# Performance work log

Measured on AMD Instinct MI355X. Metric: run time of the kernel, lower is better.

## Reference

```python
import jax, jax.numpy as jnp
import numpy as np

D_MODEL = 2048
NHEADS = 16
NOPE = 128
ROPE = 64
VDIM = 128
QLORA = 1536
KVLORA = 512
QHD = NOPE + ROPE  # 192
B, T = 1, 4096


def rms_norm(x, w):
    # torch.nn.RMSNorm with eps=None uses finfo(dtype).eps
    eps = jnp.finfo(x.dtype).eps
    var = jnp.mean(x * x, axis=-1, keepdims=True)
    return x * jax.lax.rsqrt(var + eps) * w


def rope_cos_sin(T, dim):
    freqs = 1.0 / (10000.0 ** (jnp.arange(0, dim, 2, dtype=jnp.float32) / dim))
    ang = jnp.arange(T, dtype=jnp.float32)[:, None] * freqs[None, :]  # (T, dim/2)
    return jnp.cos(ang), jnp.sin(ang)


def apply_rope(x, cos, sin):
    # interleaved RoPE: even/odd channel pairs rotated
    xe = x[..., 0::2]
    xo = x[..., 1::2]
    re = xe * cos - xo * sin
    ro = xo * cos + xe * sin
    return jnp.stack([re, ro], axis=-1).reshape(x.shape)


def setup_inputs() -> dict:
    key = jax.random.key(0)
    ks = jax.random.split(key, 6)
    s = 0.02
    return {
        "x": jax.random.normal(ks[0], (B, T, D_MODEL), jnp.float32),
        "Wqa": jax.random.normal(ks[1], (D_MODEL, QLORA), jnp.float32) * s,
        "q_ln_w": jnp.ones((QLORA,), jnp.float32),
        "Wqb": jax.random.normal(ks[2], (QLORA, NHEADS * QHD), jnp.float32) * s,
        "Wkva": jax.random.normal(ks[3], (D_MODEL, KVLORA + ROPE), jnp.float32) * s,
        "kv_ln_w": jnp.ones((KVLORA,), jnp.float32),
        "Wkvb": jax.random.normal(ks[4], (KVLORA, NHEADS * (NOPE + VDIM)), jnp.float32) * s,
        "Wo": jax.random.normal(ks[5], (NHEADS * VDIM, D_MODEL), jnp.float32) * s,
    }


def reference(x, Wqa, q_ln_w, Wqb, Wkva, kv_ln_w, Wkvb, Wo):
    Bx, Tx, _ = x.shape
    cos, sin = rope_cos_sin(Tx, ROPE)  # (T, ROPE/2)

    # Low-rank Q path
    q = rms_norm(x @ Wqa, q_ln_w) @ Wqb
    q = q.reshape(Bx, Tx, NHEADS, QHD).transpose(0, 2, 1, 3)  # (B,H,T,QHD)
    q_nope = q[..., :NOPE]
    q_rope = apply_rope(q[..., NOPE:], cos, sin)  # (B,H,T,ROPE)

    # Compressed KV path + shared rope key
    kv = x @ Wkva
    kv_c = kv[..., :KVLORA]  # (B,T,KVLORA) latent cache
    k_rope = apply_rope(kv[..., KVLORA:], cos, sin)  # (B,T,ROPE), head-shared

    kvb = (rms_norm(kv_c, kv_ln_w) @ Wkvb).reshape(Bx, Tx, NHEADS, NOPE + VDIM)
    k_nope = kvb[..., :NOPE].transpose(0, 2, 1, 3)  # (B,H,T,NOPE)
    v = kvb[..., NOPE:].transpose(0, 2, 1, 3)       # (B,H,T,VDIM)

    # Scores split into nope part + head-shared rope part (avoids expanding k_rope to H heads)
    scale = 1.0 / jnp.sqrt(jnp.float32(QHD))
    s = jnp.einsum('bhqd,bhkd->bhqk', q_nope, k_nope)
    s = s + jnp.einsum('bhqd,bkd->bhqk', q_rope, k_rope)
    s = s * scale

    mask = jnp.tril(jnp.ones((Tx, Tx), dtype=bool))
    s = jnp.where(mask, s, -jnp.inf)
    a = jax.nn.softmax(s, axis=-1)

    o = jnp.einsum('bhqk,bhkd->bhqd', a, v)
    o = o.transpose(0, 2, 1, 3).reshape(Bx, Tx, NHEADS * VDIM)
    return o @ Wo
```

## Files before the change

### kernel.cpp

```cpp
#include <hip/hip_runtime.h>
#include <hip/hip_bf16.h>

typedef __attribute__((ext_vector_type(8))) short short8;
typedef __attribute__((ext_vector_type(4))) float f32x4;

#define GLDS16(gp, lp)                                                         \
  __builtin_amdgcn_global_load_lds(                                            \
      (const __attribute__((address_space(1))) void*)(gp),                     \
      (__attribute__((address_space(3))) void*)(lp), 16, 0, 0)

static __device__ __forceinline__ unsigned int pack_bf16(float a, float b) {
  __hip_bfloat16 ba = __float2bfloat16(a), bb = __float2bfloat16(b);
  unsigned short ua = *reinterpret_cast<unsigned short*>(&ba);
  unsigned short ub = *reinterpret_cast<unsigned short*>(&bb);
  return (unsigned int)ua | ((unsigned int)ub << 16);
}

static __device__ __forceinline__ int xcd_swz(int linear, int nwg) {
  return (linear & 7) * (nwg >> 3) + (linear >> 3);
}

__global__ __launch_bounds__(256) void cast_bf16_kernel(
    const float* __restrict__ in, __hip_bfloat16* __restrict__ out, int n4)
{
  int i = blockIdx.x * 256 + threadIdx.x;
  if (i < n4) {
    float4 v = ((const float4*)in)[i];
    out[(size_t)i * 4 + 0] = __float2bfloat16(v.x);
    out[(size_t)i * 4 + 1] = __float2bfloat16(v.y);
    out[(size_t)i * 4 + 2] = __float2bfloat16(v.z);
    out[(size_t)i * 4 + 3] = __float2bfloat16(v.w);
  }
}

__global__ void transpose_cast_kernel(const float* __restrict__ in,
                                      __hip_bfloat16* __restrict__ out,
                                      int K, int N, int Npad)
{
  __shared__ float tile[32][33];
  int n0 = blockIdx.x * 32, k0 = blockIdx.y * 32;
  int tx = threadIdx.x, ty = threadIdx.y;
  #pragma unroll
  for (int i = ty; i < 32; i += 8) {
    int k = k0 + i, n = n0 + tx;
    tile[i][tx] = (n < N) ? in[(size_t)k * N + n] : 0.f;
  }
  __syncthreads();
  #pragma unroll
  for (int i = ty; i < 32; i += 8) {
    int n = n0 + i, k = k0 + tx;
    if (n < Npad) out[(size_t)n * K + k] = __float2bfloat16(tile[tx][i]);
  }
}

__global__ void rope_tab_kernel(float* __restrict__ cs, float* __restrict__ sn)
{
  int t = blockIdx.x, i = threadIdx.x;
  float freq = powf(10000.f, -2.f * (float)i / 64.f);
  float ang = (float)t * freq;
  cs[t * 32 + i] = cosf(ang);
  sn[t * 32 + i] = sinf(ang);
}

#define GEMM_MAIN(A, BT, Kdim)                                                 \
  __shared__ __hip_bfloat16 As[128 * 32];                                      \
  __shared__ __hip_bfloat16 Bs[128 * 32];                                      \
  const int tid = threadIdx.x;                                                 \
  const int wave = tid >> 6, lane = tid & 63;                                  \
  const int wr = wave >> 1, wc = wave & 1;                                     \
  const int lq = lane & 15, grp = lane >> 4;                                   \
  const int nwg = gridDim.x * gridDim.y;                                       \
  const int orig = xcd_swz(blockIdx.y * gridDim.x + blockIdx.x, nwg);          \
  const int row0 = (orig / gridDim.x) * 128;                                   \
  const int col0 = (orig % gridDim.x) * 128;                                   \
  const f32x4 z4 = {0.f, 0.f, 0.f, 0.f};                                       \
  f32x4 acc[4][4];                                                             \
  _Pragma("unroll") for (int i = 0; i < 4; i++)                                \
      _Pragma("unroll") for (int j = 0; j < 4; j++) acc[i][j] = z4;            \
  for (int k0 = 0; k0 < (Kdim); k0 += 32) {                                    \
    _Pragma("unroll") for (int i = 0; i < 2; i++) {                            \
      const int t = wave + 4 * i;                                              \
      const int c = t * 64 + lane;                                             \
      const int cr = c >> 2;                                                   \
      const int ko = (c & 3) << 3;                                             \
      GLDS16((A) + (size_t)(row0 + cr) * (Kdim) + (k0 + ko), (char*)As + t * 1024); \
      GLDS16((BT) + (size_t)(col0 + cr) * (Kdim) + (k0 + ko), (char*)Bs + t * 1024);\
    }                                                                          \
    __syncthreads();                                                           \
    short8 af[4], bfr[4];                                                      \
    _Pragma("unroll") for (int mm = 0; mm < 4; mm++)                           \
      af[mm] = *(const short8*)((const short*)As + ((wr * 64 + mm * 16 + lq) * 32 + grp * 8)); \
    _Pragma("unroll") for (int nn = 0; nn < 4; nn++)                           \
      bfr[nn] = *(const short8*)((const short*)Bs + ((wc * 64 + nn * 16 + lq) * 32 + grp * 8));\
    _Pragma("unroll") for (int mm = 0; mm < 4; mm++)                           \
      _Pragma("unroll") for (int nn = 0; nn < 4; nn++)                         \
        acc[mm][nn] = __builtin_amdgcn_mfma_f32_16x16x32_bf16(af[mm], bfr[nn], acc[mm][nn], 0, 0, 0); \
    __syncthreads();                                                           \
  }

__global__ __launch_bounds__(256) void gemm_down_kernel(
    const __hip_bfloat16* __restrict__ A,
    const __hip_bfloat16* __restrict__ BT,
    float* __restrict__ q_lat, float* __restrict__ kvout)
{
  GEMM_MAIN(A, BT, 2048)
  #pragma unroll
  for (int mm = 0; mm < 4; mm++)
    #pragma unroll
    for (int nn = 0; nn < 4; nn++) {
      const int row = row0 + wr * 64 + mm * 16 + grp * 4;
      const int col = col0 + wc * 64 + nn * 16 + lq;
      float* Cp = (col < 1536) ? (q_lat + (size_t)row * 1536 + col)
                               : (kvout + (size_t)row * 640 + (col - 1536));
      const size_t ld = (col < 1536) ? 1536 : 640;
      #pragma unroll
      for (int rr = 0; rr < 4; rr++) Cp[(size_t)rr * ld] = acc[mm][nn][rr];
    }
}

#define GEMM256_MAIN(Aptr, BTptr, Kdim)                                        \
  __shared__ __align__(16) char Ab[2][32768];                                  \
  __shared__ __align__(16) char Bb[2][32768];                                  \
  const int tid = threadIdx.x;                                                 \
  const int wid = tid >> 6, lane = tid & 63;                                   \
  const int wm = wid >> 2, wn = wid & 3;                                       \
  const int lq = lane & 15, grp = lane >> 4;                                   \
  const int nwg = gridDim.x * gridDim.y;                                       \
  const int orig = xcd_swz(blockIdx.y * gridDim.x + blockIdx.x, nwg);          \
  const int row0 = (orig / gridDim.x) * 256;                                   \
  const int col0 = (orig % gridDim.x) * 256;                                   \
  const size_t K2 = (size_t)(Kdim) * 2;                                        \
  const char* pa[4]; const char* pb[4]; int ldst[4];                           \
  _Pragma("unroll") for (int i = 0; i < 4; i++) {                              \
    int L = i * 8192 + tid * 16;                                               \
    int r = L >> 7;                                                            \
    int csw = (L & 127) ^ ((r & 7) << 4);                                      \
    ldst[i] = L;                                                               \
    pa[i] = (const char*)(Aptr) + (size_t)(row0 + r) * K2 + csw;               \
    pb[i] = (const char*)(BTptr) + (size_t)(col0 + r) * K2 + csw;              \
  }                                                                            \
  const int xm = (lq & 7) << 4;                                                \
  const f32x4 z4 = {0.f, 0.f, 0.f, 0.f};                                       \
  f32x4 acc[8][4];                                                             \
  _Pragma("unroll") for (int i = 0; i < 8; i++)                                \
    _Pragma("unroll") for (int j = 0; j < 4; j++) acc[i][j] = z4;              \
  const int nt = (Kdim) >> 6;                                                  \
  _Pragma("unroll") for (int i = 0; i < 4; i++) {                              \
    GLDS16(pa[i], &Ab[0][0] + ldst[i]);                                        \
    GLDS16(pb[i], &Bb[0][0] + ldst[i]);                                        \
  }                                                                            \
  for (int t = 0; t < nt; ++t) {                                               \
    const int b = t & 1;                                                       \
    if (t + 1 < nt) {                                                          \
      const size_t koff = (size_t)(t + 1) * 128;                               \
      _Pragma("unroll") for (int i = 0; i < 4; i++) {                          \
        GLDS16(pa[i] + koff, &Ab[b ^ 1][0] + ldst[i]);                         \
        GLDS16(pb[i] + koff, &Bb[b ^ 1][0] + ldst[i]);                         \
      }                                                                        \
      asm volatile("s_waitcnt vmcnt(8)" ::: "memory");                         \
    } else {                                                                   \
      asm volatile("s_waitcnt vmcnt(0)" ::: "memory");                         \
    }                                                                          \
    __builtin_amdgcn_sched_barrier(0);                                         \
    __builtin_amdgcn_s_barrier();             \
    __builtin_amdgcn_sched_barrier(0);                                         \
    const char* Ar = &Ab[b][0];                                                \
    const char* Br = &Bb[b][0];                                                \
    short8 bfr[4][2];                                                          \
    _Pragma("unroll") for (int n = 0; n < 4; n++)                              \
      _Pragma("unroll") for (int ks = 0; ks < 2; ks++)                         \
        bfr[n][ks] = *(const short8*)(Br + (wn * 64 + n * 16 + lq) * 128 +     \
                                      ((ks * 64 + grp * 16) ^ xm));            \
    _Pragma("unroll") for (int mh = 0; mh < 4; mh++) {                         \
      short8 af[2][2];                                                         \
      _Pragma("unroll") for (int mi = 0; mi < 2; mi++)                         \
        _Pragma("unroll") for (int ks = 0; ks < 2; ks++)                       \
          af[mi][ks] = *(const short8*)(Ar + (wm * 128 + (mh * 2 + mi) * 16 + lq) * 128 + \
                                        ((ks * 64 + grp * 16) ^ xm));          \
      __builtin_amdgcn_s_setprio(1);                                           \
      _Pragma("unroll") for (int mi = 0; mi < 2; mi++)                         \
        _Pragma("unroll") for (int n = 0; n < 4; n++)                          \
          _Pragma("unroll") for (int ks = 0; ks < 2; ks++)                     \
            acc[mh * 2 + mi][n] = __builtin_amdgcn_mfma_f32_16x16x32_bf16(     \
                af[mi][ks], bfr[n][ks], acc[mh * 2 + mi][n], 0, 0, 0);         \
      __builtin_amdgcn_s_setprio(0);                                           \
    }                                                                          \
    __builtin_amdgcn_sched_barrier(0);                                         \
    __builtin_amdgcn_s_barrier();             \
    __builtin_amdgcn_sched_barrier(0);                                         \
  }

__global__ __launch_bounds__(512, 2) void gemm256_bt_kernel(
    const __hip_bfloat16* __restrict__ A,
    const __hip_bfloat16* __restrict__ BT,
    float* __restrict__ C, int N, int K)
{
  GEMM256_MAIN(A, BT, K)
  #pragma unroll
  for (int m = 0; m < 8; m++)
    #pragma unroll
    for (int n = 0; n < 4; n++) {
      const int row = row0 + wm * 128 + m * 16 + grp * 4;
      const int col = col0 + wn * 64 + n * 16 + lq;
      float* Cp = C + (size_t)row * N + col;
      #pragma unroll
      for (int rr = 0; rr < 4; rr++) Cp[(size_t)rr * N] = acc[m][n][rr];
    }
}

__global__ __launch_bounds__(512, 2) void gemm256_qup_kernel(
    const __hip_bfloat16* __restrict__ A,
    const __hip_bfloat16* __restrict__ BT,
    __hip_bfloat16* __restrict__ Qh,
    const float* __restrict__ cs_tab, const float* __restrict__ sn_tab, int K)
{
  GEMM256_MAIN(A, BT, K)
  const float scale = 0.10411654209f;
  #pragma unroll
  for (int m = 0; m < 8; m++)
    #pragma unroll
    for (int n = 0; n < 4; n++) {
      const int col = col0 + wn * 64 + n * 16 + lq;
      const int h = col / 192;
      const int d = col - h * 192;
      const bool is_rope = (d >= 128);
      const int i = (d - 128) >> 1;
      const float sgn = (d & 1) ? 1.f : -1.f;
      #pragma unroll
      for (int rr = 0; rr < 4; rr++) {
        const int t = row0 + wm * 128 + m * 16 + grp * 4 + rr;
        float val = acc[m][n][rr];
        float partner = __shfl_xor(val, 1);
        float outv = val;
        if (is_rope) {
          float c = cs_tab[t * 32 + i];
          float s = sn_tab[t * 32 + i];
          outv = val * c + sgn * partner * s;
        }
        Qh[((size_t)h * 4096 + t) * 192 + d] = __float2bfloat16(outv * scale);
      }
    }
}

__global__ __launch_bounds__(512, 2) void gemm256_kvup_kernel(
    const __hip_bfloat16* __restrict__ A,
    const __hip_bfloat16* __restrict__ BT,
    __hip_bfloat16* __restrict__ Kh,
    __hip_bfloat16* __restrict__ Vt, int K)
{
  GEMM256_MAIN(A, BT, K)
  #pragma unroll
  for (int m = 0; m < 8; m++)
    #pragma unroll
    for (int n = 0; n < 4; n++) {
      const int col = col0 + wn * 64 + n * 16 + lq;
      const int h = col >> 8;
      const int j = col & 255;
      const int t0 = row0 + wm * 128 + m * 16 + grp * 4;
      if (j < 128) {
        #pragma unroll
        for (int rr = 0; rr < 4; rr++)
          Kh[((size_t)h * 4096 + t0 + rr) * 192 + j] = __float2bfloat16(acc[m][n][rr]);
      } else {
        const int vd = j - 128;
        uint2 w;
        w.x = pack_bf16(acc[m][n][0], acc[m][n][1]);
        w.y = pack_bf16(acc[m][n][2], acc[m][n][3]);
        *(uint2*)(Vt + ((size_t)h * 128 + vd) * 4096 + t0) = w;
      }
    }
}

__global__ __launch_bounds__(256) void rmsnorm2_kernel(
    const float* __restrict__ q_lat, const float* __restrict__ kv,
    const float* __restrict__ qw, const float* __restrict__ kvw,
    __hip_bfloat16* __restrict__ q_ln, __hip_bfloat16* __restrict__ kv_ln,
    const float* __restrict__ cs_tab, const float* __restrict__ sn_tab,
    __hip_bfloat16* __restrict__ Kh)
{
  const int b = blockIdx.x;
  const bool isq = (b < 4096);
  const int row = isq ? b : b - 4096;
  const int ld = isq ? 1536 : 640;
  const int W = isq ? 1536 : 512;
  const float* x = (isq ? q_lat : kv) + (size_t)row * ld;
  const float* w = isq ? qw : kvw;
  __hip_bfloat16* out = (isq ? q_ln : kv_ln) + (size_t)row * W;
  const int tid = threadIdx.x;
  const int wave = tid >> 6, lane = tid & 63;
  float ss = 0.f;
  for (int i = tid; i < W; i += 256) { float v = x[i]; ss += v * v; }
  #pragma unroll
  for (int o = 32; o; o >>= 1) ss += __shfl_xor(ss, o);
  __shared__ float red[4];
  __shared__ float stot;
  if (lane == 0) red[wave] = ss;
  __syncthreads();
  if (tid == 0) stot = red[0] + red[1] + red[2] + red[3];
  __syncthreads();
  const float rstd = rsqrtf(stot / (float)W + 1.1920929e-7f);
  for (int i = tid; i < W; i += 256)
    out[i] = __float2bfloat16(x[i] * rstd * w[i]);
  if (!isq) {
    const int t = row;
    for (int e = tid; e < 512; e += 256) {
      int h = e >> 5, i = e & 31;
      float c = cs_tab[t * 32 + i], s = sn_tab[t * 32 + i];
      float xe = x[512 + 2 * i];
      float xo = x[512 + 2 * i + 1];
      size_t base = ((size_t)h * 4096 + t) * 192 + 128 + 2 * i;
      Kh[base]     = __float2bfloat16(xe * c - xo * s);
      Kh[base + 1] = __float2bfloat16(xo * c + xe * s);
    }
  }
}

__global__ __launch_bounds__(256, 2) void flash_attn_kernel(
    const __hip_bfloat16* __restrict__ Qh,
    const __hip_bfloat16* __restrict__ Kh,
    const __hip_bfloat16* __restrict__ Vt,
    __hip_bfloat16* __restrict__ Obf)
{
  __shared__ __align__(16) char Klds[2][24576];
  __shared__ __align__(16) char Vlds[2][16384];

  const int hw = blockIdx.x;
  const int rest = hw >> 3;
  const int h = (hw & 7) + 8 * (rest & 1);
  const int p = rest >> 1;

  const int wave = threadIdx.x >> 6;
  const int lane = threadIdx.x & 63;
  const int lq = lane & 15;
  const int grp = lane >> 4;
  const int qb_[2] = {(63 - p) * 64 + wave * 16,
                      p * 64 + wave * 16};
  const int kendA = qb_[0] + 16;
  const int kendB = qb_[1] + 16;
  const int nt = 64 - p;

  const char* Kh_ = (const char*)(Kh + (size_t)h * 4096 * 192);
  const char* Vh_ = (const char*)(Vt + (size_t)h * 128 * 4096);
  const short* Qh_ = (const short*)Qh + (size_t)h * 4096 * 192;

  int kbase[6], vbase[4];
  #pragma unroll
  for (int i = 0; i < 6; i++) {
    int L = (wave * 6 + i) * 1024 + lane * 16;
    int r = L / 384, c = L - r * 384;
    int swb = (r & 3) | (((r >> 3) & 1) << 2);
    kbase[i] = r * 384 + (c ^ (swb << 4));
  }
  #pragma unroll
  for (int i = 0; i < 4; i++) {
    int L = (wave * 4 + i) * 1024 + lane * 16;
    int r = L >> 7, c = L & 127;
    vbase[i] = r * 8192 + (c ^ ((r & 7) << 4));
  }

  short8 qf[2][6];
  #pragma unroll
  for (int f = 0; f < 2; f++)
    #pragma unroll
    for (int d = 0; d < 6; d++)
      qf[f][d] = *(const short8*)(Qh_ + (size_t)(qb_[f] + lq) * 192 + d * 32 + grp * 8);

  const f32x4 z4 = {0.f, 0.f, 0.f, 0.f};
  f32x4 o_acc[2][8];
  #pragma unroll
  for (int f = 0; f < 2; f++)
    #pragma unroll
    for (int v = 0; v < 8; v++) o_acc[f][v] = z4;
  float m[2] = {-1e30f, -1e30f};
  float lsum[2] = {0.f, 0.f};

  const int krow_l = ((lq >> 2) << 3) + (lq & 3);
  const int kxm = ((lq & 3) | (((lq >> 2) & 1) << 2)) << 4;
  const int vxm = (lq & 7) << 4;

  {
    #pragma unroll
    for (int i = 0; i < 6; i++) GLDS16(Kh_ + kbase[i], Klds[0] + (wave * 6 + i) * 1024);
    #pragma unroll
    for (int i = 0; i < 4; i++) GLDS16(Vh_ + vbase[i], Vlds[0] + (wave * 4 + i) * 1024);
  }

  for (int t = 0; t < nt; t++) {
    __syncthreads();
    if (t + 1 < nt) {
      const char* Kp = Kh_ + (size_t)(t + 1) * 64 * 384;
      const char* Vp = Vh_ + (size_t)(t + 1) * 128;
      char* Kd = Klds[(t + 1) & 1];
      char* Vd = Vlds[(t + 1) & 1];
      #pragma unroll
      for (int i = 0; i < 6; i++) GLDS16(Kp + kbase[i], Kd + (wave * 6 + i) * 1024);
      #pragma unroll
      for (int i = 0; i < 4; i++) GLDS16(Vp + vbase[i], Vd + (wave * 4 + i) * 1024);
    }
    const char* Kb = Klds[t & 1];
    const char* Vb = Vlds[t & 1];
    const int ks = t * 64;

    #pragma unroll
    for (int h2 = 0; h2 < 2; h2++) {
      const int ks32 = ks + h2 * 32;
      if (ks32 >= kendA) continue;
      const bool act1 = (ks32 < kendB);

      f32x4 st[2][2];
      #pragma unroll
      for (int kt = 0; kt < 2; kt++) {
        const int row = h2 * 32 + krow_l + kt * 4;
        short8 kf[6];
        #pragma unroll
        for (int d = 0; d < 6; d++)
          kf[d] = *(const short8*)(Kb + row * 384 + ((d * 64 + grp * 16) ^ kxm));
        #pragma unroll
        for (int f = 0; f < 2; f++) {
          if (f == 1 && !act1) continue;
          f32x4 acc = z4;
          #pragma unroll
          for (int d = 0; d < 6; d++)
            acc = __builtin_amdgcn_mfma_f32_16x16x32_bf16(kf[d], qf[f][d], acc, 0, 0, 0);
          st[f][kt] = acc;
        }
      }

      short8 vf[8];
      #pragma unroll
      for (int v = 0; v < 8; v++)
        vf[v] = *(const short8*)(Vb + (v * 16 + lq) * 128 + ((h2 * 64 + grp * 16) ^ vxm));

      #pragma unroll
      for (int f = 0; f < 2; f++) {
        if (f == 1 && !act1) continue;
        const int qg = qb_[f] + lq;
        const bool need_mask = (ks32 + 31 > qb_[f]);
        if (need_mask) {
          #pragma unroll
          for (int kt = 0; kt < 2; kt++)
            #pragma unroll
            for (int r = 0; r < 4; r++) {
              int key = ks32 + grp * 8 + kt * 4 + r;
              if (key > qg) st[f][kt][r] = -1e30f;
            }
        }
        float tmax = fmaxf(fmaxf(fmaxf(st[f][0][0], st[f][0][1]), fmaxf(st[f][0][2], st[f][0][3])),
                           fmaxf(fmaxf(st[f][1][0], st[f][1][1]), fmaxf(st[f][1][2], st[f][1][3])));
        tmax = fmaxf(tmax, __shfl_xor(tmax, 16));
        tmax = fmaxf(tmax, __shfl_xor(tmax, 32));
        if (!__all(tmax <= m[f] + 11.5416f)) {
          float mnew = fmaxf(m[f], tmax);
          float alpha = exp2f(m[f] - mnew);
          m[f] = mnew;
          lsum[f] *= alpha;
          float a0 = __shfl(alpha, grp * 4 + 0);
          float a1 = __shfl(alpha, grp * 4 + 1);
          float a2 = __shfl(alpha, grp * 4 + 2);
          float a3 = __shfl(alpha, grp * 4 + 3);
          #pragma unroll
          for (int v = 0; v < 8; v++) {
            o_acc[f][v][0] *= a0; o_acc[f][v][1] *= a1;
            o_acc[f][v][2] *= a2; o_acc[f][v][3] *= a3;
          }
        }
        float p00 = exp2f(st[f][0][0] - m[f]), p01 = exp2f(st[f][0][1] - m[f]);
        float p02 = exp2f(st[f][0][2] - m[f]), p03 = exp2f(st[f][0][3] - m[f]);
        float p10 = exp2f(st[f][1][0] - m[f]), p11 = exp2f(st[f][1][1] - m[f]);
        float p12 = exp2f(st[f][1][2] - m[f]), p13 = exp2f(st[f][1][3] - m[f]);
        lsum[f] += ((p00 + p01) + (p02 + p03)) + ((p10 + p11) + (p12 + p13));
        union { unsigned int u[4]; short8 s8; } pu;
        pu.u[0] = pack_bf16(p00, p01);
        pu.u[1] = pack_bf16(p02, p03);
        pu.u[2] = pack_bf16(p10, p11);
        pu.u[3] = pack_bf16(p12, p13);
        short8 pa = pu.s8;
        #pragma unroll
        for (int v = 0; v < 8; v++)
          o_acc[f][v] = __builtin_amdgcn_mfma_f32_16x16x32_bf16(pa, vf[v], o_acc[f][v], 0, 0, 0);
      }
    }
  }

  #pragma unroll
  for (int f = 0; f < 2; f++) {
    float ls = lsum[f];
    ls += __shfl_xor(ls, 16);
    ls += __shfl_xor(ls, 32);
    float linv = 1.f / ls;
    float l0 = __shfl(linv, grp * 4 + 0);
    float l1 = __shfl(linv, grp * 4 + 1);
    float l2 = __shfl(linv, grp * 4 + 2);
    float l3 = __shfl(linv, grp * 4 + 3);
    const int qb = qb_[f];
    #pragma unroll
    for (int v = 0; v < 8; v++) {
      int col = h * 128 + v * 16 + lq;
      Obf[(size_t)(qb + grp * 4 + 0) * 2048 + col] = __float2bfloat16(o_acc[f][v][0] * l0);
      Obf[(size_t)(qb + grp * 4 + 1) * 2048 + col] = __float2bfloat16(o_acc[f][v][1] * l1);
      Obf[(size_t)(qb + grp * 4 + 2) * 2048 + col] = __float2bfloat16(o_acc[f][v][2] * l2);
      Obf[(size_t)(qb + grp * 4 + 3) * 2048 + col] = __float2bfloat16(o_acc[f][v][3] * l3);
    }
  }
}

extern "C" void kernel_launch(void* const* d_in, const int* in_sizes, int n_in,
                              void* d_out, int out_size, void* d_ws, size_t ws_size,
                              hipStream_t stream)
{
  (void)in_sizes; (void)n_in; (void)out_size; (void)ws_size;
  const float* x     = (const float*)d_in[0];
  const float* Wqa   = (const float*)d_in[1];
  const float* qlnw  = (const float*)d_in[2];
  const float* Wqb   = (const float*)d_in[3];
  const float* Wkva  = (const float*)d_in[4];
  const float* kvlnw = (const float*)d_in[5];
  const float* Wkvb  = (const float*)d_in[6];
  const float* Wo    = (const float*)d_in[7];
  float* out = (float*)d_out;
  char* ws = (char*)d_ws;

  size_t off = 0;
  auto take = [&](size_t bytes) {
    char* p = ws + off;
    off += (bytes + 255) & ~(size_t)255;
    return p;
  };

  __hip_bfloat16* x_bf   = (__hip_bfloat16*)take((size_t)4096 * 2048 * 2);
  __hip_bfloat16* WdownT = (__hip_bfloat16*)take((size_t)2176 * 2048 * 2);
  __hip_bfloat16* WqbT   = (__hip_bfloat16*)take((size_t)3072 * 1536 * 2);
  __hip_bfloat16* WkvbT  = (__hip_bfloat16*)take((size_t)4096 * 512 * 2);
  __hip_bfloat16* WoT    = (__hip_bfloat16*)take((size_t)2048 * 2048 * 2);
  char* regA             = take((size_t)4096 * 1536 * 4);
  float* kv              = (float*)take((size_t)4096 * 640 * 4);
  __hip_bfloat16* q_ln   = (__hip_bfloat16*)take((size_t)4096 * 1536 * 2);
  __hip_bfloat16* kv_ln  = (__hip_bfloat16*)take((size_t)4096 * 512 * 2);
  float* cs_tab          = (float*)take((size_t)4096 * 32 * 4);
  float* sn_tab          = (float*)take((size_t)4096 * 32 * 4);
  __hip_bfloat16* Khp    = (__hip_bfloat16*)take((size_t)16 * 4096 * 192 * 2);
  __hip_bfloat16* Vtp    = (__hip_bfloat16*)take((size_t)16 * 128 * 4096 * 2);
  __hip_bfloat16* o_bf   = (__hip_bfloat16*)take((size_t)4096 * 2048 * 2);

  float* q_lat = (float*)regA;
  __hip_bfloat16* Qh = (__hip_bfloat16*)regA;

  cast_bf16_kernel<<<dim3(8192), 256, 0, stream>>>(x, x_bf, 2097152);
  transpose_cast_kernel<<<dim3(48, 64), dim3(32, 8), 0, stream>>>(Wqa, WdownT, 2048, 1536, 1536);
  transpose_cast_kernel<<<dim3(20, 64), dim3(32, 8), 0, stream>>>(Wkva, WdownT + (size_t)1536 * 2048, 2048, 576, 640);
  transpose_cast_kernel<<<dim3(96, 48), dim3(32, 8), 0, stream>>>(Wqb, WqbT, 1536, 3072, 3072);
  transpose_cast_kernel<<<dim3(128, 16), dim3(32, 8), 0, stream>>>(Wkvb, WkvbT, 512, 4096, 4096);
  transpose_cast_kernel<<<dim3(64, 64), dim3(32, 8), 0, stream>>>(Wo, WoT, 2048, 2048, 2048);
  rope_tab_kernel<<<dim3(4096), 32, 0, stream>>>(cs_tab, sn_tab);

  gemm_down_kernel<<<dim3(17, 32), 256, 0, stream>>>(x_bf, WdownT, q_lat, kv);

  rmsnorm2_kernel<<<dim3(8192), 256, 0, stream>>>(q_lat, kv, qlnw, kvlnw, q_ln, kv_ln,
                                                  cs_tab, sn_tab, Khp);

  gemm256_qup_kernel<<<dim3(12, 16), 512, 0, stream>>>(q_ln, WqbT, Qh, cs_tab, sn_tab, 1536);
  gemm256_kvup_kernel<<<dim3(16, 16), 512, 0, stream>>>(kv_ln, WkvbT, Khp, Vtp, 512);

  flash_attn_kernel<<<dim3(512), 256, 0, stream>>>(Qh, Khp, Vtp, o_bf);

  gemm256_bt_kernel<<<dim3(8, 16), 512, 0, stream>>>(o_bf, WoT, out, 2048, 2048);
}
```

Baseline: 466.3 us.

## Merge prep and up-projection launches, use 128-tile GEMM for output projection

Folds the RoPE table build into the cast kernel and the five weight transposes into one launch. The Q-up and KV-up GEMMs now run as a single 448-block kernel. The output projection switches from the 256-tile double-buffered GEMM (128 blocks) to the simpler 128-tile GEMM (512 blocks), trading per-block efficiency for better CU coverage. Fewer launches cut launch overhead and tail gaps between small kernels.

```diff
diff --git a/kernel.cpp b/kernel.cpp
--- a/kernel.cpp
+++ b/kernel.cpp
@@ -20,8 +20,9 @@
   return (linear & 7) * (nwg >> 3) + (linear >> 3);
 }
 
-__global__ __launch_bounds__(256) void cast_bf16_kernel(
-    const float* __restrict__ in, __hip_bfloat16* __restrict__ out, int n4)
+__global__ __launch_bounds__(256) void cast_rope_kernel(
+    const float* __restrict__ in, __hip_bfloat16* __restrict__ out, int n4,
+    float* __restrict__ cs, float* __restrict__ sn)
 {
   int i = blockIdx.x * 256 + threadIdx.x;
   if (i < n4) {
@@ -31,14 +32,33 @@
     out[(size_t)i * 4 + 2] = __float2bfloat16(v.z);
     out[(size_t)i * 4 + 3] = __float2bfloat16(v.w);
   }
-}
-
-__global__ void transpose_cast_kernel(const float* __restrict__ in,
-                                      __hip_bfloat16* __restrict__ out,
-                                      int K, int N, int Npad)
+  if (blockIdx.x < 4096 && threadIdx.x < 32) {
+    int t = blockIdx.x, j = threadIdx.x;
+    float freq = powf(10000.f, -2.f * (float)j / 64.f);
+    float ang = (float)t * freq;
+    cs[t * 32 + j] = cosf(ang);
+    sn[t * 32 + j] = sinf(ang);
+  }
+}
+
+__global__ void transpose_all_kernel(
+    const float* __restrict__ Wqa, const float* __restrict__ Wkva,
+    const float* __restrict__ Wqb, const float* __restrict__ Wkvb,
+    const float* __restrict__ Wo,
+    __hip_bfloat16* __restrict__ WdownT, __hip_bfloat16* __restrict__ WqbT,
+    __hip_bfloat16* __restrict__ WkvbT, __hip_bfloat16* __restrict__ WoT)
 {
   __shared__ float tile[32][33];
-  int n0 = blockIdx.x * 32, k0 = blockIdx.y * 32;
+  int b = blockIdx.x;
+  const float* in;
+  __hip_bfloat16* outp;
+  int K, N, Npad, gx;
+  if (b < 3072)        { in = Wqa;  outp = WdownT;                        K = 2048; N = 1536; Npad = 1536; gx = 48; }
+  else if (b < 4352)   { b -= 3072; in = Wkva; outp = WdownT + (size_t)1536 * 2048; K = 2048; N = 576;  Npad = 640;  gx = 20; }
+  else if (b < 8960)   { b -= 4352; in = Wqb;  outp = WqbT;               K = 1536; N = 3072; Npad = 3072; gx = 96; }
+  else if (b < 11008)  { b -= 8960; in = Wkvb; outp = WkvbT;              K = 512;  N = 4096; Npad = 4096; gx = 128; }
+  else                 { b -= 11008; in = Wo;  outp = WoT;                K = 2048; N = 2048; Npad = 2048; gx = 64; }
+  int n0 = (b % gx) * 32, k0 = (b / gx) * 32;
   int tx = threadIdx.x, ty = threadIdx.y;
   #pragma unroll
   for (int i = ty; i < 32; i += 8) {
@@ -49,17 +69,8 @@
   #pragma unroll
   for (int i = ty; i < 32; i += 8) {
     int n = n0 + i, k = k0 + tx;
-    if (n < Npad) out[(size_t)n * K + k] = __float2bfloat16(tile[tx][i]);
-  }
-}
-
-__global__ void rope_tab_kernel(float* __restrict__ cs, float* __restrict__ sn)
-{
-  int t = blockIdx.x, i = threadIdx.x;
-  float freq = powf(10000.f, -2.f * (float)i / 64.f);
-  float ang = (float)t * freq;
-  cs[t * 32 + i] = cosf(ang);
-  sn[t * 32 + i] = sinf(ang);
+    if (n < Npad) outp[(size_t)n * K + k] = __float2bfloat16(tile[tx][i]);
+  }
 }
 
 #define GEMM_MAIN(A, BT, Kdim)                                                 \
@@ -98,6 +109,24 @@
     __syncthreads();                                                           \
   }
 
+__global__ __launch_bounds__(256) void gemm_bt_kernel(
+    const __hip_bfloat16* __restrict__ A,
+    const __hip_bfloat16* __restrict__ BT,
+    float* __restrict__ C, int M, int N, int K)
+{
+  GEMM_MAIN(A, BT, K)
+  #pragma unroll
+  for (int mm = 0; mm < 4; mm++)
+    #pragma unroll
+    for (int nn = 0; nn < 4; nn++) {
+      const int row = row0 + wr * 64 + mm * 16 + grp * 4;
+      const int col = col0 + wc * 64 + nn * 16 + lq;
+      float* Cp = C + (size_t)row * N + col;
+      #pragma unroll
+      for (int rr = 0; rr < 4; rr++) Cp[(size_t)rr * N] = acc[mm][nn][rr];
+    }
+}
+
 __global__ __launch_bounds__(256) void gemm_down_kernel(
     const __hip_bfloat16* __restrict__ A,
     const __hip_bfloat16* __restrict__ BT,
@@ -118,157 +147,138 @@
     }
 }
 
-#define GEMM256_MAIN(Aptr, BTptr, Kdim)                                        \
-  __shared__ __align__(16) char Ab[2][32768];                                  \
-  __shared__ __align__(16) char Bb[2][32768];                                  \
-  const int tid = threadIdx.x;                                                 \
-  const int wid = tid >> 6, lane = tid & 63;                                   \
-  const int wm = wid >> 2, wn = wid & 3;                                       \
-  const int lq = lane & 15, grp = lane >> 4;                                   \
-  const int nwg = gridDim.x * gridDim.y;                                       \
-  const int orig = xcd_swz(blockIdx.y * gridDim.x + blockIdx.x, nwg);          \
-  const int row0 = (orig / gridDim.x) * 256;                                   \
-  const int col0 = (orig % gridDim.x) * 256;                                   \
-  const size_t K2 = (size_t)(Kdim) * 2;                                        \
-  const char* pa[4]; const char* pb[4]; int ldst[4];                           \
-  _Pragma("unroll") for (int i = 0; i < 4; i++) {                              \
-    int L = i * 8192 + tid * 16;                                               \
-    int r = L >> 7;                                                            \
-    int csw = (L & 127) ^ ((r & 7) << 4);                                      \
-    ldst[i] = L;                                                               \
-    pa[i] = (const char*)(Aptr) + (size_t)(row0 + r) * K2 + csw;               \
-    pb[i] = (const char*)(BTptr) + (size_t)(col0 + r) * K2 + csw;              \
-  }                                                                            \
-  const int xm = (lq & 7) << 4;                                                \
-  const f32x4 z4 = {0.f, 0.f, 0.f, 0.f};                                       \
-  f32x4 acc[8][4];                                                             \
-  _Pragma("unroll") for (int i = 0; i < 8; i++)                                \
-    _Pragma("unroll") for (int j = 0; j < 4; j++) acc[i][j] = z4;              \
-  const int nt = (Kdim) >> 6;                                                  \
-  _Pragma("unroll") for (int i = 0; i < 4; i++) {                              \
-    GLDS16(pa[i], &Ab[0][0] + ldst[i]);                                        \
-    GLDS16(pb[i], &Bb[0][0] + ldst[i]);                                        \
-  }                                                                            \
-  for (int t = 0; t < nt; ++t) {                                               \
-    const int b = t & 1;                                                       \
-    if (t + 1 < nt) {                                                          \
-      const size_t koff = (size_t)(t + 1) * 128;                               \
-      _Pragma("unroll") for (int i = 0; i < 4; i++) {                          \
-        GLDS16(pa[i] + koff, &Ab[b ^ 1][0] + ldst[i]);                         \
-        GLDS16(pb[i] + koff, &Bb[b ^ 1][0] + ldst[i]);                         \
+#define GEMM256_BODY(Aptr, BTptr, Kdim, ROW0, COL0)                            \
+    const size_t K2 = (size_t)(Kdim) * 2;                                      \
+    const char* pa[4]; const char* pb[4]; int ldst[4];                         \
+    _Pragma("unroll") for (int i = 0; i < 4; i++) {                            \
+      int L = i * 8192 + tid * 16;                                             \
+      int r = L >> 7;                                                          \
+      int csw = (L & 127) ^ ((r & 7) << 4);                                    \
+      ldst[i] = L;                                                             \
+      pa[i] = (const char*)(Aptr) + (size_t)((ROW0) + r) * K2 + csw;           \
+      pb[i] = (const char*)(BTptr) + (size_t)((COL0) + r) * K2 + csw;          \
+    }                                                                          \
+    f32x4 acc[8][4];                                                           \
+    _Pragma("unroll") for (int i = 0; i < 8; i++)                              \
+      _Pragma("unroll") for (int j = 0; j < 4; j++) acc[i][j] = z4;            \
+    const int nt = (Kdim) >> 6;                                                \
+    _Pragma("unroll") for (int i = 0; i < 4; i++) {                            \
+      GLDS16(pa[i], &Ab[0][0] + ldst[i]);                                      \
+      GLDS16(pb[i], &Bb[0][0] + ldst[i]);                                      \
+    }                                                                          \
+    for (int t = 0; t < nt; ++t) {                                             \
+      const int b = t & 1;                                                     \
+      if (t + 1 < nt) {                                                        \
+        const size_t koff = (size_t)(t + 1) * 128;                             \
+        _Pragma("unroll") for (int i = 0; i < 4; i++) {                        \
+          GLDS16(pa[i] + koff, &Ab[b ^ 1][0] + ldst[i]);                       \
+          GLDS16(pb[i] + koff, &Bb[b ^ 1][0] + ldst[i]);                       \
+        }                                                                      \
+        asm volatile("s_waitcnt vmcnt(8)" ::: "memory");                       \
+      } else {                                                                 \
+        asm volatile("s_waitcnt vmcnt(0)" ::: "memory");                       \
       }                                                                        \
-      asm volatile("s_waitcnt vmcnt(8)" ::: "memory");                         \
-    } else {                                                                   \
-      asm volatile("s_waitcnt vmcnt(0)" ::: "memory");                         \
-    }                                                                          \
-    __builtin_amdgcn_sched_barrier(0);                                         \
-    __builtin_amdgcn_s_barrier();             \
-    __builtin_amdgcn_sched_barrier(0);                                         \
-    const char* Ar = &Ab[b][0];                                                \
-    const char* Br = &Bb[b][0];                                                \
-    short8 bfr[4][2];                                                          \
-    _Pragma("unroll") for (int n = 0; n < 4; n++)                              \
-      _Pragma("unroll") for (int ks = 0; ks < 2; ks++)                         \
-        bfr[n][ks] = *(const short8*)(Br + (wn * 64 + n * 16 + lq) * 128 +     \
-                                      ((ks * 64 + grp * 16) ^ xm));            \
-    _Pragma("unroll") for (int mh = 0; mh < 4; mh++) {                         \
-      short8 af[2][2];                                                         \
-      _Pragma("unroll") for (int mi = 0; mi < 2; mi++)                         \
+      __builtin_amdgcn_sched_barrier(0);                                       \
+      __builtin_amdgcn_s_barrier();                                            \
+      __builtin_amdgcn_sched_barrier(0);                                       \
+      const char* Ar = &Ab[b][0];                                              \
+      const char* Br = &Bb[b][0];                                              \
+      short8 bfr[4][2];                                                        \
+      _Pragma("unroll") for (int n = 0; n < 4; n++)                            \
         _Pragma("unroll") for (int ks = 0; ks < 2; ks++)                       \
-          af[mi][ks] = *(const short8*)(Ar + (wm * 128 + (mh * 2 + mi) * 16 + lq) * 128 + \
+          bfr[n][ks] = *(const short8*)(Br + (wn * 64 + n * 16 + lq) * 128 +   \
                                         ((ks * 64 + grp * 16) ^ xm));          \
-      __builtin_amdgcn_s_setprio(1);                                           \
-      _Pragma("unroll") for (int mi = 0; mi < 2; mi++)                         \
-        _Pragma("unroll") for (int n = 0; n < 4; n++)                          \
+      _Pragma("unroll") for (int mh = 0; mh < 4; mh++) {                       \
+        short8 af[2][2];                                                       \
+        _Pragma("unroll") for (int mi = 0; mi < 2; mi++)                       \
           _Pragma("unroll") for (int ks = 0; ks < 2; ks++)                     \
-            acc[mh * 2 + mi][n] = __builtin_amdgcn_mfma_f32_16x16x32_bf16(     \
-                af[mi][ks], bfr[n][ks], acc[mh * 2 + mi][n], 0, 0, 0);         \
-      __builtin_amdgcn_s_setprio(0);                                           \
-    }                                                                          \
-    __builtin_amdgcn_sched_barrier(0);                                         \
-    __builtin_amdgcn_s_barrier();             \
-    __builtin_amdgcn_sched_barrier(0);                                         \
-  }
-
-__global__ __launch_bounds__(512, 2) void gemm256_bt_kernel(
-    const __hip_bfloat16* __restrict__ A,
-    const __hip_bfloat16* __restrict__ BT,
-    float* __restrict__ C, int N, int K)
-{
-  GEMM256_MAIN(A, BT, K)
-  #pragma unroll
-  for (int m = 0; m < 8; m++)
-    #pragma unroll
-    for (int n = 0; n < 4; n++) {
-      const int row = row0 + wm * 128 + m * 16 + grp * 4;
-      const int col = col0 + wn * 64 + n * 16 + lq;
-      float* Cp = C + (size_t)row * N + col;
-      #pragma unroll
-      for (int rr = 0; rr < 4; rr++) Cp[(size_t)rr * N] = acc[m][n][rr];
-    }
-}
-
-__global__ __launch_bounds__(512, 2) void gemm256_qup_kernel(
-    const __hip_bfloat16* __restrict__ A,
-    const __hip_bfloat16* __restrict__ BT,
+            af[mi][ks] = *(const short8*)(Ar + (wm * 128 + (mh * 2 + mi) * 16 + lq) * 128 + \
+                                          ((ks * 64 + grp * 16) ^ xm));        \
+        __builtin_amdgcn_s_setprio(1);                                         \
+        _Pragma("unroll") for (int mi = 0; mi < 2; mi++)                       \
+          _Pragma("unroll") for (int n = 0; n < 4; n++)                        \
+            _Pragma("unroll") for (int ks = 0; ks < 2; ks++)                   \
+              acc[mh * 2 + mi][n] = __builtin_amdgcn_mfma_f32_16x16x32_bf16(   \
+                  af[mi][ks], bfr[n][ks], acc[mh * 2 + mi][n], 0, 0, 0);       \
+        __builtin_amdgcn_s_setprio(0);                                         \
+      }                                                                        \
+      __builtin_amdgcn_sched_barrier(0);                                       \
+      __builtin_amdgcn_s_barrier();                                            \
+      __builtin_amdgcn_sched_barrier(0);                                       \
+    }
+
+__global__ __launch_bounds__(512, 2) void gemm256_up_kernel(
+    const __hip_bfloat16* __restrict__ q_ln, const __hip_bfloat16* __restrict__ WqbT,
     __hip_bfloat16* __restrict__ Qh,
-    const float* __restrict__ cs_tab, const float* __restrict__ sn_tab, int K)
-{
-  GEMM256_MAIN(A, BT, K)
-  const float scale = 0.10411654209f;
-  #pragma unroll
-  for (int m = 0; m < 8; m++)
-    #pragma unroll
-    for (int n = 0; n < 4; n++) {
-      const int col = col0 + wn * 64 + n * 16 + lq;
-      const int h = col / 192;
-      const int d = col - h * 192;
-      const bool is_rope = (d >= 128);
-      const int i = (d - 128) >> 1;
-      const float sgn = (d & 1) ? 1.f : -1.f;
-      #pragma unroll
-      for (int rr = 0; rr < 4; rr++) {
-        const int t = row0 + wm * 128 + m * 16 + grp * 4 + rr;
-        float val = acc[m][n][rr];
-        float partner = __shfl_xor(val, 1);
-        float outv = val;
-        if (is_rope) {
-          float c = cs_tab[t * 32 + i];
-          float s = sn_tab[t * 32 + i];
-          outv = val * c + sgn * partner * s;
+    const float* __restrict__ cs_tab, const float* __restrict__ sn_tab,
+    const __hip_bfloat16* __restrict__ kv_ln, const __hip_bfloat16* __restrict__ WkvbT,
+    __hip_bfloat16* __restrict__ Kh, __hip_bfloat16* __restrict__ Vt)
+{
+  __shared__ __align__(16) char Ab[2][32768];
+  __shared__ __align__(16) char Bb[2][32768];
+  const int tid = threadIdx.x;
+  const int wid = tid >> 6, lane = tid & 63;
+  const int wm = wid >> 2, wn = wid & 3;
+  const int lq = lane & 15, grp = lane >> 4;
+  const int xm = (lq & 7) << 4;
+  const f32x4 z4 = {0.f, 0.f, 0.f, 0.f};
+  const int sw = xcd_swz(blockIdx.x, 448);
+
+  if (sw < 192) {
+    const int row0 = (sw / 12) * 256;
+    const int col0 = (sw % 12) * 256;
+    GEMM256_BODY(q_ln, WqbT, 1536, row0, col0)
+    const float scale = 0.10411654209f;
+    #pragma unroll
+    for (int m = 0; m < 8; m++)
+      #pragma unroll
+      for (int n = 0; n < 4; n++) {
+        const int col = col0 + wn * 64 + n * 16 + lq;
+        const int h = col / 192;
+        const int d = col - h * 192;
+        const bool is_rope = (d >= 128);
+        const int i = (d - 128) >> 1;
+        const float sgn = (d & 1) ? 1.f : -1.f;
+        #pragma unroll
+        for (int rr = 0; rr < 4; rr++) {
+          const int t = row0 + wm * 128 + m * 16 + grp * 4 + rr;
+          float val = acc[m][n][rr];
+          float partner = __shfl_xor(val, 1);
+          float outv = val;
+          if (is_rope) {
+            float c = cs_tab[t * 32 + i];
+            float s = sn_tab[t * 32 + i];
+            outv = val * c + sgn * partner * s;
+          }
+          Qh[((size_t)h * 4096 + t) * 192 + d] = __float2bfloat16(outv * scale);
         }
-        Qh[((size_t)h * 4096 + t) * 192 + d] = __float2bfloat16(outv * scale);
       }
-    }
-}
-
-__global__ __launch_bounds__(512, 2) void gemm256_kvup_kernel(
-    const __hip_bfloat16* __restrict__ A,
-    const __hip_bfloat16* __restrict__ BT,
-    __hip_bfloat16* __restrict__ Kh,
-    __hip_bfloat16* __restrict__ Vt, int K)
-{
-  GEMM256_MAIN(A, BT, K)
-  #pragma unroll
-  for (int m = 0; m < 8; m++)
-    #pragma unroll
-    for (int n = 0; n < 4; n++) {
-      const int col = col0 + wn * 64 + n * 16 + lq;
-      const int h = col >> 8;
-      const int j = col & 255;
-      const int t0 = row0 + wm * 128 + m * 16 + grp * 4;
-      if (j < 128) {
-        #pragma unroll
-        for (int rr = 0; rr < 4; rr++)
-          Kh[((size_t)h * 4096 + t0 + rr) * 192 + j] = __float2bfloat16(acc[m][n][rr]);
-      } else {
-        const int vd = j - 128;
-        uint2 w;
-        w.x = pack_bf16(acc[m][n][0], acc[m][n][1]);
-        w.y = pack_bf16(acc[m][n][2], acc[m][n][3]);
-        *(uint2*)(Vt + ((size_t)h * 128 + vd) * 4096 + t0) = w;
+  } else {
+    const int bb = sw - 192;
+    const int row0 = (bb / 16) * 256;
+    const int col0 = (bb % 16) * 256;
+    GEMM256_BODY(kv_ln, WkvbT, 512, row0, col0)
+    #pragma unroll
+    for (int m = 0; m < 8; m++)
+      #pragma unroll
+      for (int n = 0; n < 4; n++) {
+        const int col = col0 + wn * 64 + n * 16 + lq;
+        const int h = col >> 8;
+        const int j = col & 255;
+        const int t0 = row0 + wm * 128 + m * 16 + grp * 4;
+        if (j < 128) {
+          #pragma unroll
+          for (int rr = 0; rr < 4; rr++)
+            Kh[((size_t)h * 4096 + t0 + rr) * 192 + j] = __float2bfloat16(acc[m][n][rr]);
+        } else {
+          const int vd = j - 128;
+          uint2 w;
+          w.x = pack_bf16(acc[m][n][0], acc[m][n][1]);
+          w.y = pack_bf16(acc[m][n][2], acc[m][n][3]);
+          *(uint2*)(Vt + ((size_t)h * 128 + vd) * 4096 + t0) = w;
+        }
       }
-    }
+  }
 }
 
 __global__ __launch_bounds__(256) void rmsnorm2_kernel(
@@ -545,23 +555,19 @@
   float* q_lat = (float*)regA;
   __hip_bfloat16* Qh = (__hip_bfloat16*)regA;
 
-  cast_bf16_kernel<<<dim3(8192), 256, 0, stream>>>(x, x_bf, 2097152);
-  transpose_cast_kernel<<<dim3(48, 64), dim3(32, 8), 0, stream>>>(Wqa, WdownT, 2048, 1536, 1536);
-  transpose_cast_kernel<<<dim3(20, 64), dim3(32, 8), 0, stream>>>(Wkva, WdownT + (size_t)1536 * 2048, 2048, 576, 640);
-  transpose_cast_kernel<<<dim3(96, 48), dim3(32, 8), 0, stream>>>(Wqb, WqbT, 1536, 3072, 3072);
-  transpose_cast_kernel<<<dim3(128, 16), dim3(32, 8), 0, stream>>>(Wkvb, WkvbT, 512, 4096, 4096);
-  transpose_cast_kernel<<<dim3(64, 64), dim3(32, 8), 0, stream>>>(Wo, WoT, 2048, 2048, 2048);
-  rope_tab_kernel<<<dim3(4096), 32, 0, stream>>>(cs_tab, sn_tab);
+  cast_rope_kernel<<<dim3(8192), 256, 0, stream>>>(x, x_bf, 2097152, cs_tab, sn_tab);
+  transpose_all_kernel<<<dim3(15104), dim3(32, 8), 0, stream>>>(
+      Wqa, Wkva, Wqb, Wkvb, Wo, WdownT, WqbT, WkvbT, WoT);
 
   gemm_down_kernel<<<dim3(17, 32), 256, 0, stream>>>(x_bf, WdownT, q_lat, kv);
 
   rmsnorm2_kernel<<<dim3(8192), 256, 0, stream>>>(q_lat, kv, qlnw, kvlnw, q_ln, kv_ln,
                                                   cs_tab, sn_tab, Khp);
 
-  gemm256_qup_kernel<<<dim3(12, 16), 512, 0, stream>>>(q_ln, WqbT, Qh, cs_tab, sn_tab, 1536);
-  gemm256_kvup_kernel<<<dim3(16, 16), 512, 0, stream>>>(kv_ln, WkvbT, Khp, Vtp, 512);
+  gemm256_up_kernel<<<dim3(448), 512, 0, stream>>>(q_ln, WqbT, Qh, cs_tab, sn_tab,
+                                                   kv_ln, WkvbT, Khp, Vtp);
 
   flash_attn_kernel<<<dim3(512), 256, 0, stream>>>(Qh, Khp, Vtp, o_bf);
 
-  gemm256_bt_kernel<<<dim3(8, 16), 512, 0, stream>>>(o_bf, WoT, out, 2048, 2048);
-}
+  gemm_bt_kernel<<<dim3(16, 32), 256, 0, stream>>>(o_bf, WoT, out, 4096, 2048, 2048);
+}
```

Result: slower. 487.7 us (+4.6%).
